# Kernel optimization log

Hardware: AMD Instinct MI355X
Metric: run time of the kernel (lower is better)

The kernel has to match this reference:

```python
import jax, jax.numpy as jnp
import numpy as np

N = 100000   # total atoms
M = 12       # neighbors per atom
C = 2000     # crystals
ORIG = 92    # original atom feature len
NBR = 41     # edge (Gaussian distance) feature len
F = 64       # atom_fea_len
H = 128      # h_fea_len
NCONV = 3
EPS = 1e-5


def setup_inputs() -> dict:
    key = jax.random.key(0)
    ks = jax.random.split(key, 12)
    def w(k, shape, fan_in):
        return (jax.random.normal(k, shape, jnp.float32) / np.sqrt(fan_in)).astype(jnp.float32)
    inp = {}
    inp["atom_fea"] = jax.random.normal(ks[0], (N, ORIG), jnp.float32)
    inp["nbr_fea"] = jax.random.normal(ks[1], (N, M, NBR), jnp.float32)
    inp["nbr_fea_idx"] = jax.random.randint(ks[2], (N, M), 0, N)
    inp["crystal_ids"] = jnp.sort(jax.random.randint(ks[3], (N,), 0, C))
    inp["emb_W"] = w(ks[4], (ORIG, F), ORIG)
    inp["emb_b"] = jnp.zeros((F,), jnp.float32)
    inp["conv_W"] = w(ks[5], (NCONV, 2 * F + NBR, 2 * F), 2 * F + NBR)
    inp["conv_b"] = jnp.zeros((NCONV, 2 * F), jnp.float32)
    inp["bn1_g"] = jnp.ones((NCONV, 2 * F), jnp.float32)
    inp["bn1_b"] = jnp.zeros((NCONV, 2 * F), jnp.float32)
    inp["bn2_g"] = jnp.ones((NCONV, F), jnp.float32)
    inp["bn2_b"] = jnp.zeros((NCONV, F), jnp.float32)
    inp["W3_W"] = w(ks[6], (F, F), F)
    inp["W3_b"] = jnp.zeros((F,), jnp.float32)
    inp["fc_W"] = w(ks[7], (F, H), F)
    inp["fc_b"] = jnp.zeros((H,), jnp.float32)
    inp["out_W"] = w(ks[8], (H, 1), H)
    inp["out_b"] = jnp.zeros((1,), jnp.float32)
    return inp


def _bn(x, g, b):
    # BatchNorm1d in training mode: batch mean, biased variance
    m = jnp.mean(x, axis=0)
    v = jnp.var(x, axis=0)
    return (x - m) * jax.lax.rsqrt(v + EPS) * g + b


def _seg_mean(x, ids, num):
    s = jax.ops.segment_sum(x, ids, num_segments=num)          # [num, F]
    cnt = jax.ops.segment_sum(jnp.ones((x.shape[0], 1), x.dtype), ids, num_segments=num)
    return s / jnp.maximum(cnt, 1.0)


def _conv_layer(x, nbr_fea, nbr_idx, W, b, g1, b1, g2, b2):
    n, m = nbr_idx.shape
    atom_nbr = x[nbr_idx]                                      # [N, M, F] gather
    self_fea = jnp.broadcast_to(x[:, None, :], (n, m, x.shape[1]))
    total = jnp.concatenate([self_fea, atom_nbr, nbr_fea], axis=2)  # [N, M, 2F+NBR]
    gated = total @ W + b                                      # [N, M, 2F]
    gated = _bn(gated.reshape(-1, 2 * F), g1, b1).reshape(n, m, 2 * F)
    nbr_filter = jax.nn.sigmoid(gated[..., :F])
    nbr_core = jnp.tanh(gated[..., F:])
    nbr_sumed = jnp.sum(nbr_filter * nbr_core, axis=1)          # [N, F]
    nbr_sumed = _bn(nbr_sumed, g2, b2)
    return jnp.tanh(x + nbr_sumed)


def reference(atom_fea, nbr_fea, nbr_fea_idx, crystal_ids,
              emb_W, emb_b, conv_W, conv_b, bn1_g, bn1_b, bn2_g, bn2_b,
              W3_W, W3_b, fc_W, fc_b, out_W, out_b):
    x = atom_fea @ emb_W + emb_b                               # [N, F]
    for i in range(NCONV):
        x = _conv_layer(x, nbr_fea, nbr_fea_idx, conv_W[i], conv_b[i],
                        bn1_g[i], bn1_b[i], bn2_g[i], bn2_b[i])
    # pooling(): per-crystal mean expanded back to each atom
    crys_mean = _seg_mean(x, crystal_ids, C)                   # [C, F]
    v_ = crys_mean[crystal_ids]                                # [N, F]
    c = jnp.tanh(v_ @ W3_W + W3_b)                             # [N, F]
    a = jax.nn.sigmoid(jnp.sum(x * c, axis=1, keepdims=True))  # [N, 1]
    crys_fea = _seg_mean(a * x, crystal_ids, C)                # [C, F]
    crys_fea = jax.nn.softplus(crys_fea @ fc_W + fc_b)         # [C, H]
    out = crys_fea @ out_W + out_b                             # [C, 1]
    return out, x
```

## Files before the change

### kernel.cpp

```cpp
#include <hip/hip_runtime.h>
#include <hip/hip_bf16.h>


#define NA    100000
#define MN    12
#define NC    2000
#define ORIGF 92
#define NBRF  41
#define FD    64
#define NBLK  3125
#define EPSF  1e-5f

#define REP28(X) X(0)X(1)X(2)X(3)X(4)X(5)X(6)X(7)X(8)X(9)X(10)X(11)X(12)X(13)X(14)X(15)X(16)X(17)X(18)X(19)X(20)X(21)X(22)X(23)X(24)X(25)X(26)X(27)
#define REP41(X) X(0)X(1)X(2)X(3)X(4)X(5)X(6)X(7)X(8)X(9)X(10)X(11)X(12)X(13)X(14)X(15)X(16)X(17)X(18)X(19)X(20)X(21)X(22)X(23)X(24)X(25)X(26)X(27)X(28)X(29)X(30)X(31)X(32)X(33)X(34)X(35)X(36)X(37)X(38)X(39)X(40)
#define REP64(X) X(0)X(1)X(2)X(3)X(4)X(5)X(6)X(7)X(8)X(9)X(10)X(11)X(12)X(13)X(14)X(15)X(16)X(17)X(18)X(19)X(20)X(21)X(22)X(23)X(24)X(25)X(26)X(27)X(28)X(29)X(30)X(31)X(32)X(33)X(34)X(35)X(36)X(37)X(38)X(39)X(40)X(41)X(42)X(43)X(44)X(45)X(46)X(47)X(48)X(49)X(50)X(51)X(52)X(53)X(54)X(55)X(56)X(57)X(58)X(59)X(60)X(61)X(62)X(63)

typedef const float* fp;

__device__ __forceinline__ float rlf(float v, int q){
  return __int_as_float(__builtin_amdgcn_readlane(__float_as_int(v), q));
}
__device__ __forceinline__ float fsig(float z){
  z = fminf(fmaxf(z, -30.f), 30.f);
  return 1.f / (1.f + __expf(-z));
}
__device__ __forceinline__ float ftanh(float z){
  z = fminf(fmaxf(z, -15.f), 15.f);
  float e = __expf(2.f * z);
  return (e - 1.f) / (e + 1.f);
}

__global__ void zero_kernel(float* __restrict__ p, int n){
  for (int i = blockIdx.x * blockDim.x + threadIdx.x; i < n; i += gridDim.x * blockDim.x)
    p[i] = 0.f;
}

__global__ __launch_bounds__(256, 2) void emb_kernel(
    fp __restrict__ af, fp __restrict__ W, fp __restrict__ b,
    float* __restrict__ x)
{
  const int lane = threadIdx.x & 63, w = threadIdx.x >> 6;
#define EA(k) float wa##k = W[k * FD + lane];
  REP64(EA)
#undef EA
#define EB(k) float wb##k = W[(k + 64) * FD + lane];
  REP28(EB)
#undef EB
  const float bias = b[lane];
  const int base = blockIdx.x * 32 + w * 8;
  #pragma unroll 1
  for (int it = 0; it < 8; ++it){
    const int i = base + it;
    float ev0 = af[i * ORIGF + lane];
    float ev1 = (lane < 28) ? af[i * ORIGF + 64 + lane] : 0.f;
    float acc = bias;
#define FA(k) acc = fmaf(rlf(ev0, k), wa##k, acc);
    REP64(FA)
#undef FA
#define FB(k) acc = fmaf(rlf(ev1, k), wb##k, acc);
    REP28(FB)
#undef FB
    x[i * FD + lane] = acc;
  }
}

__global__ __launch_bounds__(256, 4) void stw_kernel(
    const float* __restrict__ xin, fp __restrict__ W, fp __restrict__ bias,
    float* __restrict__ out)
{
  const int lane = threadIdx.x & 63, w = threadIdx.x >> 6;
  const int ch = (w & 1) * 64 + lane;
#define SW(k) float wv##k = W[k * 128 + ch];
  REP64(SW)
#undef SW
  const float bb = bias ? bias[ch] : 0.f;
  const int base = blockIdx.x * 32 + (w >> 1) * 16;
  #pragma unroll 1
  for (int it = 0; it < 16; ++it){
    const int i = base + it;
    float xv = xin[i * FD + lane];
    float acc = bb;
#define SF(k) acc = fmaf(rlf(xv, k), wv##k, acc);
    REP64(SF)
#undef SF
    out[i * 128 + ch] = acc;
  }
}

__global__ __launch_bounds__(256, 2) void edge_stats_kernel(
    const float* __restrict__ S, const float* __restrict__ T,
    fp __restrict__ nbr, const int* __restrict__ idx,
    fp __restrict__ We, float* __restrict__ p1)
{
  const int lane = threadIdx.x & 63, w = threadIdx.x >> 6;
  const int clo = lane, chi = lane + 64;
#define DW(q) float wlo##q = We[q * 128 + clo], whi##q = We[q * 128 + chi];
  REP41(DW)
#undef DW
  float sum_lo = 0.f, ssq_lo = 0.f, sum_hi = 0.f, ssq_hi = 0.f;
  const int base = blockIdx.x * 32 + w * 8;
  #pragma unroll 1
  for (int it = 0; it < 8; ++it){
    const int i = base + it;
    const float slo = S[i * 128 + clo];
    const float shi = S[i * 128 + chi];
    int kk = (lane < MN) ? idx[i * MN + lane] : 0;
    fp nb = nbr + (size_t)i * (MN * NBRF);
    int k0 = __builtin_amdgcn_readlane(kk, 0);
    float tlo = T[k0 * 128 + clo];
    float thi = T[k0 * 128 + chi];
    float ev  = (lane < NBRF) ? nb[lane] : 0.f;
    #pragma unroll 1
    for (int j = 0; j < MN; j++){
      float tlo_n = 0.f, thi_n = 0.f, ev_n = 0.f;
      if (j + 1 < MN){
        int kn = __builtin_amdgcn_readlane(kk, j + 1);
        tlo_n = T[kn * 128 + clo];
        thi_n = T[kn * 128 + chi];
        ev_n  = (lane < NBRF) ? nb[(j + 1) * NBRF + lane] : 0.f;
      }
      float glo = slo + tlo, ghi = shi + thi;
#define EF(q) { float s_ = rlf(ev, q); glo = fmaf(s_, wlo##q, glo); ghi = fmaf(s_, whi##q, ghi); }
      REP41(EF)
#undef EF
      sum_lo += glo; ssq_lo = fmaf(glo, glo, ssq_lo);
      sum_hi += ghi; ssq_hi = fmaf(ghi, ghi, ssq_hi);
      tlo = tlo_n; thi = thi_n; ev = ev_n;
    }
  }
  __shared__ float red[4 * 512];
  red[w * 512 + 2 * clo    ] = sum_lo;
  red[w * 512 + 2 * clo + 1] = ssq_lo;
  red[w * 512 + 2 * chi    ] = sum_hi;
  red[w * 512 + 2 * chi + 1] = ssq_hi;
  __syncthreads();
  const int t = threadIdx.x;
  const int ch = t & 127, which = t >> 7;
  float v = 0.f;
  #pragma unroll
  for (int ww = 0; ww < 4; ++ww) v += red[ww * 512 + 2 * ch + which];
  p1[blockIdx.x * 256 + t] = v;
}

__global__ __launch_bounds__(256, 2) void edge_stats_store_kernel(
    const float* __restrict__ S, const float* __restrict__ T,
    fp __restrict__ nbr, const int* __restrict__ idx,
    fp __restrict__ We, float* __restrict__ p1, float* __restrict__ gated)
{
  const int lane = threadIdx.x & 63, w = threadIdx.x >> 6;
  const int clo = lane, chi = lane + 64;
#define DW(q) float wlo##q = We[q * 128 + clo], whi##q = We[q * 128 + chi];
  REP41(DW)
#undef DW
  float sum_lo = 0.f, ssq_lo = 0.f, sum_hi = 0.f, ssq_hi = 0.f;
  const int base = blockIdx.x * 32 + w * 8;
  #pragma unroll 1
  for (int it = 0; it < 8; ++it){
    const int i = base + it;
    const float slo = S[i * 128 + clo];
    const float shi = S[i * 128 + chi];
    int kk = (lane < MN) ? idx[i * MN + lane] : 0;
    fp nb = nbr + (size_t)i * (MN * NBRF);
    float* gb = gated + (((size_t)i * MN) << 7) + 2 * lane;
    int k0 = __builtin_amdgcn_readlane(kk, 0);
    float tlo = T[k0 * 128 + clo];
    float thi = T[k0 * 128 + chi];
    float ev  = (lane < NBRF) ? nb[lane] : 0.f;
    #pragma unroll 1
    for (int j = 0; j < MN; j++){
      float tlo_n = 0.f, thi_n = 0.f, ev_n = 0.f;
      if (j + 1 < MN){
        int kn = __builtin_amdgcn_readlane(kk, j + 1);
        tlo_n = T[kn * 128 + clo];
        thi_n = T[kn * 128 + chi];
        ev_n  = (lane < NBRF) ? nb[(j + 1) * NBRF + lane] : 0.f;
      }
      float glo = slo + tlo, ghi = shi + thi;
#define EF(q) { float s_ = rlf(ev, q); glo = fmaf(s_, wlo##q, glo); ghi = fmaf(s_, whi##q, ghi); }
      REP41(EF)
#undef EF
      *(float2*)(gb + ((size_t)j << 7)) = make_float2(glo, ghi);
      sum_lo += glo; ssq_lo = fmaf(glo, glo, ssq_lo);
      sum_hi += ghi; ssq_hi = fmaf(ghi, ghi, ssq_hi);
      tlo = tlo_n; thi = thi_n; ev = ev_n;
    }
  }
  __shared__ float red[4 * 512];
  red[w * 512 + 2 * clo    ] = sum_lo;
  red[w * 512 + 2 * clo + 1] = ssq_lo;
  red[w * 512 + 2 * chi    ] = sum_hi;
  red[w * 512 + 2 * chi + 1] = ssq_hi;
  __syncthreads();
  const int t = threadIdx.x;
  const int ch = t & 127, which = t >> 7;
  float v = 0.f;
  #pragma unroll
  for (int ww = 0; ww < 4; ++ww) v += red[ww * 512 + 2 * ch + which];
  p1[blockIdx.x * 256 + t] = v;
}

__global__ __launch_bounds__(256, 4) void edge_apply_load_kernel(
    const float* __restrict__ gated, const float* __restrict__ ss1,
    float* __restrict__ ns, float* __restrict__ p2)
{
  const int lane = threadIdx.x & 63, w = threadIdx.x >> 6;
  const float sc_lo = ss1[lane],      sh_lo = ss1[128 + lane];
  const float sc_hi = ss1[64 + lane], sh_hi = ss1[192 + lane];
  float sum2 = 0.f, ssq2 = 0.f;
  const int base = blockIdx.x * 32 + w * 8;
  #pragma unroll 1
  for (int it = 0; it < 8; ++it){
    const int i = base + it;
    fp gb = gated + (((size_t)i * MN) << 7) + 2 * lane;
    float acc = 0.f;
    #pragma unroll
    for (int j = 0; j < MN; ++j){
      float2 gv = *(const float2*)(gb + ((size_t)j << 7));
      float filt = fsig(fmaf(gv.x, sc_lo, sh_lo));
      float core = ftanh(fmaf(gv.y, sc_hi, sh_hi));
      acc = fmaf(filt, core, acc);
    }
    ns[i * FD + lane] = acc;
    sum2 += acc; ssq2 = fmaf(acc, acc, ssq2);
  }
  __shared__ float red[4 * 128];
  red[w * 128 + 2 * lane    ] = sum2;
  red[w * 128 + 2 * lane + 1] = ssq2;
  __syncthreads();
  const int t = threadIdx.x;
  if (t < 128){
    const int ch = t & 63, which = t >> 6;
    float v = 0.f;
    #pragma unroll
    for (int ww = 0; ww < 4; ++ww) v += red[ww * 128 + 2 * ch + which];
    p2[blockIdx.x * 128 + t] = v;
  }
}

__global__ __launch_bounds__(256, 2) void edge_apply_kernel(
    const float* __restrict__ S, const float* __restrict__ T,
    fp __restrict__ nbr, const int* __restrict__ idx,
    fp __restrict__ We, const float* __restrict__ ss1,
    float* __restrict__ ns, float* __restrict__ p2)
{
  const int lane = threadIdx.x & 63, w = threadIdx.x >> 6;
  const int clo = lane, chi = lane + 64;
#define DW(q) float wlo##q = We[q * 128 + clo], whi##q = We[q * 128 + chi];
  REP41(DW)
#undef DW
  const float sc_lo = ss1[clo],       sh_lo = ss1[128 + clo];
  const float sc_hi = ss1[chi],       sh_hi = ss1[128 + chi];
  float sum2 = 0.f, ssq2 = 0.f;
  const int base = blockIdx.x * 32 + w * 8;
  #pragma unroll 1
  for (int it = 0; it < 8; ++it){
    const int i = base + it;
    const float slo = S[i * 128 + clo];
    const float shi = S[i * 128 + chi];
    int kk = (lane < MN) ? idx[i * MN + lane] : 0;
    fp nb = nbr + (size_t)i * (MN * NBRF);
    int k0 = __builtin_amdgcn_readlane(kk, 0);
    float tlo = T[k0 * 128 + clo];
    float thi = T[k0 * 128 + chi];
    float ev  = (lane < NBRF) ? nb[lane] : 0.f;
    float acc = 0.f;
    #pragma unroll 1
    for (int j = 0; j < MN; j++){
      float tlo_n = 0.f, thi_n = 0.f, ev_n = 0.f;
      if (j + 1 < MN){
        int kn = __builtin_amdgcn_readlane(kk, j + 1);
        tlo_n = T[kn * 128 + clo];
        thi_n = T[kn * 128 + chi];
        ev_n  = (lane < NBRF) ? nb[(j + 1) * NBRF + lane] : 0.f;
      }
      float glo = slo + tlo, ghi = shi + thi;
#define EF(q) { float s_ = rlf(ev, q); glo = fmaf(s_, wlo##q, glo); ghi = fmaf(s_, whi##q, ghi); }
      REP41(EF)
#undef EF
      float filt = fsig(fmaf(glo, sc_lo, sh_lo));
      float core = ftanh(fmaf(ghi, sc_hi, sh_hi));
      acc = fmaf(filt, core, acc);
      tlo = tlo_n; thi = thi_n; ev = ev_n;
    }
    ns[i * FD + lane] = acc;
    sum2 += acc; ssq2 = fmaf(acc, acc, ssq2);
  }
  __shared__ float red[4 * 128];
  red[w * 128 + 2 * lane    ] = sum2;
  red[w * 128 + 2 * lane + 1] = ssq2;
  __syncthreads();
  const int t = threadIdx.x;
  if (t < 128){
    const int ch = t & 63, which = t >> 6;
    float v = 0.f;
    #pragma unroll
    for (int ww = 0; ww < 4; ++ww) v += red[ww * 128 + 2 * ch + which];
    p2[blockIdx.x * 128 + t] = v;
  }
}

__global__ void reduce_rows_kernel(const float* __restrict__ p, float* __restrict__ accum,
                                   int nrows, int ncols)
{
  const int t = threadIdx.x;
  float a = 0.f;
  for (int r = blockIdx.x; r < nrows; r += gridDim.x) a += p[r * ncols + t];
  atomicAdd(&accum[t], a);
}

__global__ void finalize1_kernel(const float* __restrict__ acc, fp g, fp b,
                                 float* __restrict__ ss1)
{
  const int c = threadIdx.x;
  const float inv = 1.f / 1200000.f;
  float mean = acc[c] * inv;
  float var  = fmaxf(acc[128 + c] * inv - mean * mean, 0.f);
  float sc   = g[c] * rsqrtf(var + EPSF);
  ss1[c] = sc;
  ss1[128 + c] = b[c] - mean * sc;
}

__global__ void finalize2_kernel(const float* __restrict__ acc, fp g, fp b,
                                 float* __restrict__ ss2)
{
  const int c = threadIdx.x;
  const float inv = 1.f / 100000.f;
  float mean = acc[c] * inv;
  float var  = fmaxf(acc[64 + c] * inv - mean * mean, 0.f);
  float sc   = g[c] * rsqrtf(var + EPSF);
  ss2[c] = sc;
  ss2[64 + c] = b[c] - mean * sc;
}

__global__ __launch_bounds__(256) void bn2res_kernel(
    float* __restrict__ x, const float* __restrict__ ns,
    const float* __restrict__ ss2, float* __restrict__ xout)
{
  const int e = (blockIdx.x * 256 + threadIdx.x) * 4;
  const int c = e & 63;
  float4 xv = *(const float4*)(x + e);
  float4 nv = *(const float4*)(ns + e);
  float r0 = ftanh(fmaf(nv.x, ss2[c + 0], ss2[64 + c + 0]) + xv.x);
  float r1 = ftanh(fmaf(nv.y, ss2[c + 1], ss2[64 + c + 1]) + xv.y);
  float r2 = ftanh(fmaf(nv.z, ss2[c + 2], ss2[64 + c + 2]) + xv.z);
  float r3 = ftanh(fmaf(nv.w, ss2[c + 3], ss2[64 + c + 3]) + xv.w);
  *(float4*)(x + e) = make_float4(r0, r1, r2, r3);
  if (xout){
    *(float4*)(xout + e) = make_float4(r0, r1, r2, r3);
  }
}

__global__ __launch_bounds__(256) void pool1_kernel(
    const float* __restrict__ x, const int* __restrict__ cid,
    float* __restrict__ csum, float* __restrict__ ccnt)
{
  const int lane = threadIdx.x & 63, w = threadIdx.x >> 6;
  const int wg = blockIdx.x * 4 + w;
  const int i0 = wg * 64;
  if (i0 >= NA) return;
  const int i1 = min(i0 + 64, NA);
  int cur = -1; float acc = 0.f; int run = 0;
  for (int i = i0; i < i1; ++i){
    int cd = cid[i];
    if (cd != cur){
      if (cur >= 0){
        atomicAdd(&csum[cur * FD + lane], acc);
        if (lane == 0) atomicAdd(&ccnt[cur], (float)run);
      }
      cur = cd; acc = 0.f; run = 0;
    }
    acc += x[i * FD + lane];
    run++;
  }
  if (cur >= 0){
    atomicAdd(&csum[cur * FD + lane], acc);
    if (lane == 0) atomicAdd(&ccnt[cur], (float)run);
  }
}

__global__ void cm3_kernel(const float* __restrict__ csum, const float* __restrict__ ccnt,
                           fp W3, fp b3, float* __restrict__ c3)
{
  const int b = blockIdx.x, t = threadIdx.x;
  __shared__ float mean[64];
  float inv = 1.f / fmaxf(ccnt[b], 1.f);
  mean[t] = csum[b * FD + t] * inv;
  __syncthreads();
  float acc = b3[t];
  #pragma unroll
  for (int k = 0; k < 64; k++) acc = fmaf(mean[k], W3[k * FD + t], acc);
  c3[b * FD + t] = ftanh(acc);
}

__global__ __launch_bounds__(256) void pool2_kernel(
    const float* __restrict__ x, const int* __restrict__ cid,
    const float* __restrict__ c3, float* __restrict__ cfs)
{
  const int lane = threadIdx.x & 63, w = threadIdx.x >> 6;
  const int wg = blockIdx.x * 4 + w;
  const int i0 = wg * 64;
  if (i0 >= NA) return;
  const int i1 = min(i0 + 64, NA);
  int cur = -1; float acc = 0.f;
  for (int i = i0; i < i1; ++i){
    int cd = cid[i];
    if (cd != cur){
      if (cur >= 0) atomicAdd(&cfs[cur * FD + lane], acc);
      cur = cd; acc = 0.f;
    }
    float xv = x[i * FD + lane];
    float p = xv * c3[cd * FD + lane];
    #pragma unroll
    for (int off = 32; off; off >>= 1) p += __shfl_xor(p, off);
    acc = fmaf(fsig(p), xv, acc);
  }
  if (cur >= 0) atomicAdd(&cfs[cur * FD + lane], acc);
}

__global__ void head_kernel(const float* __restrict__ cfs, const float* __restrict__ ccnt,
                            fp fcW, fp fcb, fp oW, fp ob,
                            float* __restrict__ outp)
{
  const int b = blockIdx.x, t = threadIdx.x;
  __shared__ float row[64];
  __shared__ float red[128];
  float inv = 1.f / fmaxf(ccnt[b], 1.f);
  if (t < 64) row[t] = cfs[b * FD + t] * inv;
  __syncthreads();
  float acc = fcb[t];
  #pragma unroll
  for (int k = 0; k < 64; k++) acc = fmaf(row[k], fcW[k * 128 + t], acc);
  float sp = (acc > 20.f) ? acc : log1pf(__expf(acc));
  red[t] = sp * oW[t];
  __syncthreads();
  for (int off = 64; off; off >>= 1){
    if (t < off) red[t] += red[t + off];
    __syncthreads();
  }
  if (t == 0) outp[b] = red[0] + ob[0];
}

static const size_t O_X    = 0;
static const size_t O_S    = 6400000;
static const size_t O_T    = 19200000;
static const size_t O_NS   = 32000000;
static const size_t O_P1   = 38400000;
static const size_t O_P2   = 39200000;
static const size_t O_SS1  = 39600000;
static const size_t O_SS2  = 39600256;
static const size_t O_G1   = 39600384;
static const size_t O_G2   = 39600640;
static const size_t O_CSUM = 39600768;
static const size_t O_CCNT = 39728768;
static const size_t O_C3   = 39730768;
static const size_t O_CFS  = 39858768;
static const size_t O_END  = 39986768;
static const size_t O_GATED= 39986768;
static const size_t O_END2 = 193586768;

extern "C" void kernel_launch(void* const* d_in, const int* in_sizes, int n_in,
                              void* d_out, int out_size, void* d_ws, size_t ws_size,
                              hipStream_t stream)
{
  (void)in_sizes; (void)n_in; (void)out_size;
  if (ws_size < O_END * sizeof(float)) return;
  const bool big = ws_size >= O_END2 * sizeof(float);

  fp atom_fea = (fp)d_in[0];
  fp nbr_fea  = (fp)d_in[1];
  const int* nbr_idx = (const int*)d_in[2];
  const int* cids    = (const int*)d_in[3];
  fp embW = (fp)d_in[4];
  fp embb = (fp)d_in[5];
  fp convW = (fp)d_in[6];
  fp convb = (fp)d_in[7];
  fp bn1g = (fp)d_in[8];
  fp bn1b = (fp)d_in[9];
  fp bn2g = (fp)d_in[10];
  fp bn2b = (fp)d_in[11];
  fp W3W  = (fp)d_in[12];
  fp W3b  = (fp)d_in[13];
  fp fcW  = (fp)d_in[14];
  fp fcb  = (fp)d_in[15];
  fp oW   = (fp)d_in[16];
  fp ob   = (fp)d_in[17];

  float* out_head = (float*)d_out;
  float* out_x    = out_head + NC;

  float* W  = (float*)d_ws;
  float* x    = W + O_X;
  float* S    = W + O_S;
  float* T    = W + O_T;
  float* ns   = W + O_NS;
  float* p1   = W + O_P1;
  float* p2   = W + O_P2;
  float* ss1  = W + O_SS1;
  float* ss2  = W + O_SS2;
  float* g1s  = W + O_G1;
  float* g2s  = W + O_G2;
  float* csum = W + O_CSUM;
  float* ccnt = W + O_CCNT;
  float* c3   = W + O_C3;
  float* cfs  = W + O_CFS;
  float* gated= W + O_GATED;

  zero_kernel<<<128, 256, 0, stream>>>(csum, 386000);

  emb_kernel<<<NBLK, 256, 0, stream>>>(atom_fea, embW, embb, x);

  for (int l = 0; l < 3; ++l){
    fp Wl = convW + (size_t)l * 169 * 128;
    stw_kernel<<<NBLK, 256, 0, stream>>>(x, Wl,            convb + l * 128, S);
    stw_kernel<<<NBLK, 256, 0, stream>>>(x, Wl + 64 * 128, (fp)nullptr,     T);
    zero_kernel<<<1, 256, 0, stream>>>(g1s, 384);
    if (big){
      edge_stats_store_kernel<<<NBLK, 256, 0, stream>>>(S, T, nbr_fea, nbr_idx, Wl + 128 * 128, p1, gated);
      reduce_rows_kernel<<<64, 256, 0, stream>>>(p1, g1s, NBLK, 256);
      finalize1_kernel<<<1, 128, 0, stream>>>(g1s, bn1g + l * 128, bn1b + l * 128, ss1);
      edge_apply_load_kernel<<<NBLK, 256, 0, stream>>>(gated, ss1, ns, p2);
    } else {
      edge_stats_kernel<<<NBLK, 256, 0, stream>>>(S, T, nbr_fea, nbr_idx, Wl + 128 * 128, p1);
      reduce_rows_kernel<<<64, 256, 0, stream>>>(p1, g1s, NBLK, 256);
      finalize1_kernel<<<1, 128, 0, stream>>>(g1s, bn1g + l * 128, bn1b + l * 128, ss1);
      edge_apply_kernel<<<NBLK, 256, 0, stream>>>(S, T, nbr_fea, nbr_idx, Wl + 128 * 128, ss1, ns, p2);
    }
    reduce_rows_kernel<<<64, 128, 0, stream>>>(p2, g2s, NBLK, 128);
    finalize2_kernel<<<1, 64, 0, stream>>>(g2s, bn2g + l * 64, bn2b + l * 64, ss2);
    bn2res_kernel<<<6250, 256, 0, stream>>>(x, ns, ss2, (l == 2) ? out_x : (float*)nullptr);
  }

  pool1_kernel<<<391, 256, 0, stream>>>(x, cids, csum, ccnt);
  cm3_kernel<<<NC, 64, 0, stream>>>(csum, ccnt, W3W, W3b, c3);
  pool2_kernel<<<391, 256, 0, stream>>>(x, cids, c3, cfs);
  head_kernel<<<NC, 128, 0, stream>>>(cfs, ccnt, fcW, fcb, oW, ob, out_head);
}
```

Measured before the change: 2.548 ms.

## Split edge GEMV channels across warps to halve registers and raise occupancy

Each wavefront in the edge stats/store kernel now handles one 64-channel half instead of both, so it keeps 41 weights in registers instead of 82. Launch bounds go from 2 to 4 blocks per SM, and each wave pair covers 16 atoms instead of 8. The gated buffer layout changes from interleaved lo/hi float2 to planar halves, and the apply kernel now reads it as two scalar loads. In exchange, the S/T gathers, index loads and lane broadcasts of edge features are now done by two waves instead of one.

```diff
diff --git a/kernel.cpp b/kernel.cpp
--- a/kernel.cpp
+++ b/kernel.cpp
@@ -142,60 +142,57 @@
   p1[blockIdx.x * 256 + t] = v;
 }
 
-__global__ __launch_bounds__(256, 2) void edge_stats_store_kernel(
+__global__ __launch_bounds__(256, 4) void edge_stats_store_kernel(
     const float* __restrict__ S, const float* __restrict__ T,
     fp __restrict__ nbr, const int* __restrict__ idx,
     fp __restrict__ We, float* __restrict__ p1, float* __restrict__ gated)
 {
   const int lane = threadIdx.x & 63, w = threadIdx.x >> 6;
-  const int clo = lane, chi = lane + 64;
-#define DW(q) float wlo##q = We[q * 128 + clo], whi##q = We[q * 128 + chi];
+  const int half = w & 1;
+  const int ch = half * 64 + lane;
+#define DW(q) float wv##q = We[q * 128 + ch];
   REP41(DW)
 #undef DW
-  float sum_lo = 0.f, ssq_lo = 0.f, sum_hi = 0.f, ssq_hi = 0.f;
-  const int base = blockIdx.x * 32 + w * 8;
+#define PIN(q) asm volatile("" : "+v"(wv##q));
+  REP41(PIN)
+#undef PIN
+  float sum = 0.f, ssq = 0.f;
+  const int base = blockIdx.x * 32 + (w >> 1) * 16;
   #pragma unroll 1
-  for (int it = 0; it < 8; ++it){
+  for (int it = 0; it < 16; ++it){
     const int i = base + it;
-    const float slo = S[i * 128 + clo];
-    const float shi = S[i * 128 + chi];
+    const float sv = S[i * 128 + ch];
     int kk = (lane < MN) ? idx[i * MN + lane] : 0;
     fp nb = nbr + (size_t)i * (MN * NBRF);
-    float* gb = gated + (((size_t)i * MN) << 7) + 2 * lane;
+    float* gb = gated + (((size_t)i * MN) << 7) + ch;
     int k0 = __builtin_amdgcn_readlane(kk, 0);
-    float tlo = T[k0 * 128 + clo];
-    float thi = T[k0 * 128 + chi];
-    float ev  = (lane < NBRF) ? nb[lane] : 0.f;
+    float tv = T[k0 * 128 + ch];
+    float ev = (lane < NBRF) ? nb[lane] : 0.f;
     #pragma unroll 1
     for (int j = 0; j < MN; j++){
-      float tlo_n = 0.f, thi_n = 0.f, ev_n = 0.f;
+      float tv_n = 0.f, ev_n = 0.f;
       if (j + 1 < MN){
         int kn = __builtin_amdgcn_readlane(kk, j + 1);
-        tlo_n = T[kn * 128 + clo];
-        thi_n = T[kn * 128 + chi];
-        ev_n  = (lane < NBRF) ? nb[(j + 1) * NBRF + lane] : 0.f;
+        tv_n = T[kn * 128 + ch];
+        ev_n = (lane < NBRF) ? nb[(j + 1) * NBRF + lane] : 0.f;
       }
-      float glo = slo + tlo, ghi = shi + thi;
-#define EF(q) { float s_ = rlf(ev, q); glo = fmaf(s_, wlo##q, glo); ghi = fmaf(s_, whi##q, ghi); }
+      float g = sv + tv;
+#define EF(q) g = fmaf(rlf(ev, q), wv##q, g);
       REP41(EF)
 #undef EF
-      *(float2*)(gb + ((size_t)j << 7)) = make_float2(glo, ghi);
-      sum_lo += glo; ssq_lo = fmaf(glo, glo, ssq_lo);
-      sum_hi += ghi; ssq_hi = fmaf(ghi, ghi, ssq_hi);
-      tlo = tlo_n; thi = thi_n; ev = ev_n;
-    }
-  }
-  __shared__ float red[4 * 512];
-  red[w * 512 + 2 * clo    ] = sum_lo;
-  red[w * 512 + 2 * clo + 1] = ssq_lo;
-  red[w * 512 + 2 * chi    ] = sum_hi;
-  red[w * 512 + 2 * chi + 1] = ssq_hi;
+      gb[(size_t)j << 7] = g;
+      sum += g; ssq = fmaf(g, g, ssq);
+      tv = tv_n; ev = ev_n;
+    }
+  }
+  __shared__ float red[4 * 128];
+  red[w * 128 + 2 * lane    ] = sum;
+  red[w * 128 + 2 * lane + 1] = ssq;
   __syncthreads();
   const int t = threadIdx.x;
-  const int ch = t & 127, which = t >> 7;
-  float v = 0.f;
-  #pragma unroll
-  for (int ww = 0; ww < 4; ++ww) v += red[ww * 512 + 2 * ch + which];
+  const int c = t & 127, which = t >> 7;
+  const int h = c >> 6, cl = c & 63;
+  float v = red[h * 128 + 2 * cl + which] + red[(h + 2) * 128 + 2 * cl + which];
   p1[blockIdx.x * 256 + t] = v;
 }
 
@@ -211,13 +208,14 @@
   #pragma unroll 1
   for (int it = 0; it < 8; ++it){
     const int i = base + it;
-    fp gb = gated + (((size_t)i * MN) << 7) + 2 * lane;
+    fp gb = gated + (((size_t)i * MN) << 7);
     float acc = 0.f;
     #pragma unroll
     for (int j = 0; j < MN; ++j){
-      float2 gv = *(const float2*)(gb + ((size_t)j << 7));
-      float filt = fsig(fmaf(gv.x, sc_lo, sh_lo));
-      float core = ftanh(fmaf(gv.y, sc_hi, sh_hi));
+      float glo = gb[(j << 7) + lane];
+      float ghi = gb[(j << 7) + 64 + lane];
+      float filt = fsig(fmaf(glo, sc_lo, sh_lo));
+      float core = ftanh(fmaf(ghi, sc_hi, sh_hi));
       acc = fmaf(filt, core, acc);
     }
     ns[i * FD + lane] = acc;
```

Measured after the change: 2.869 ms. 1.13x slower.

## Stage edge features in LDS and process four neighbors per batch

Applied to the files above, without the earlier changes.

The edge-stats kernel now copies each atom's 12x41 edge-feature block into shared memory and reads the values as LDS broadcasts, replacing per-coefficient readlane broadcasts. It processes four neighbors per inner step, issuing the four T gathers together to get more memory-level parallelism and ILP. The gated buffer layout changes from interleaved lo/hi float2 to split lo and hi halves, and the apply kernel is updated to match. The costs are higher register pressure from four accumulator pairs, and the LDS write-then-read relies only on a waitcnt with no barrier, which is fine within a single wave.

```diff
diff --git a/kernel.cpp b/kernel.cpp
--- a/kernel.cpp
+++ b/kernel.cpp
@@ -152,6 +152,7 @@
 #define DW(q) float wlo##q = We[q * 128 + clo], whi##q = We[q * 128 + chi];
   REP41(DW)
 #undef DW
+  __shared__ float elds[4][MN * NBRF];
   float sum_lo = 0.f, ssq_lo = 0.f, sum_hi = 0.f, ssq_hi = 0.f;
   const int base = blockIdx.x * 32 + w * 8;
   #pragma unroll 1
@@ -161,28 +162,43 @@
     const float shi = S[i * 128 + chi];
     int kk = (lane < MN) ? idx[i * MN + lane] : 0;
     fp nb = nbr + (size_t)i * (MN * NBRF);
-    float* gb = gated + (((size_t)i * MN) << 7) + 2 * lane;
-    int k0 = __builtin_amdgcn_readlane(kk, 0);
-    float tlo = T[k0 * 128 + clo];
-    float thi = T[k0 * 128 + chi];
-    float ev  = (lane < NBRF) ? nb[lane] : 0.f;
+    #pragma unroll
+    for (int r = 0; r < 7; ++r) elds[w][r * 64 + lane] = nb[r * 64 + lane];
+    if (lane < MN * NBRF - 448) elds[w][448 + lane] = nb[448 + lane];
+    asm volatile("s_waitcnt lgkmcnt(0)" ::: "memory");
     #pragma unroll 1
-    for (int j = 0; j < MN; j++){
-      float tlo_n = 0.f, thi_n = 0.f, ev_n = 0.f;
-      if (j + 1 < MN){
-        int kn = __builtin_amdgcn_readlane(kk, j + 1);
-        tlo_n = T[kn * 128 + clo];
-        thi_n = T[kn * 128 + chi];
-        ev_n  = (lane < NBRF) ? nb[(j + 1) * NBRF + lane] : 0.f;
-      }
-      float glo = slo + tlo, ghi = shi + thi;
-#define EF(q) { float s_ = rlf(ev, q); glo = fmaf(s_, wlo##q, glo); ghi = fmaf(s_, whi##q, ghi); }
+    for (int jg = 0; jg < MN / 4; ++jg){
+      const int j0 = jg * 4;
+      int k0 = __builtin_amdgcn_readlane(kk, j0);
+      int k1 = __builtin_amdgcn_readlane(kk, j0 + 1);
+      int k2 = __builtin_amdgcn_readlane(kk, j0 + 2);
+      int k3 = __builtin_amdgcn_readlane(kk, j0 + 3);
+      float g0lo = slo + T[k0 * 128 + clo], g0hi = shi + T[k0 * 128 + chi];
+      float g1lo = slo + T[k1 * 128 + clo], g1hi = shi + T[k1 * 128 + chi];
+      float g2lo = slo + T[k2 * 128 + clo], g2hi = shi + T[k2 * 128 + chi];
+      float g3lo = slo + T[k3 * 128 + clo], g3hi = shi + T[k3 * 128 + chi];
+      const float* eb = &elds[w][j0 * NBRF];
+#define EF(q) { float e0_ = eb[q]; float e1_ = eb[NBRF + q]; \
+                float e2_ = eb[2 * NBRF + q]; float e3_ = eb[3 * NBRF + q]; \
+                g0lo = fmaf(e0_, wlo##q, g0lo); g0hi = fmaf(e0_, whi##q, g0hi); \
+                g1lo = fmaf(e1_, wlo##q, g1lo); g1hi = fmaf(e1_, whi##q, g1hi); \
+                g2lo = fmaf(e2_, wlo##q, g2lo); g2hi = fmaf(e2_, whi##q, g2hi); \
+                g3lo = fmaf(e3_, wlo##q, g3lo); g3hi = fmaf(e3_, whi##q, g3hi); }
       REP41(EF)
 #undef EF
-      *(float2*)(gb + ((size_t)j << 7)) = make_float2(glo, ghi);
-      sum_lo += glo; ssq_lo = fmaf(glo, glo, ssq_lo);
-      sum_hi += ghi; ssq_hi = fmaf(ghi, ghi, ssq_hi);
-      tlo = tlo_n; thi = thi_n; ev = ev_n;
+      float* gb = gated + (((size_t)(i * MN + j0)) << 7);
+      gb[lane]       = g0lo; gb[64 + lane]  = g0hi;
+      gb[128 + lane] = g1lo; gb[192 + lane] = g1hi;
+      gb[256 + lane] = g2lo; gb[320 + lane] = g2hi;
+      gb[384 + lane] = g3lo; gb[448 + lane] = g3hi;
+      sum_lo += g0lo; ssq_lo = fmaf(g0lo, g0lo, ssq_lo);
+      sum_hi += g0hi; ssq_hi = fmaf(g0hi, g0hi, ssq_hi);
+      sum_lo += g1lo; ssq_lo = fmaf(g1lo, g1lo, ssq_lo);
+      sum_hi += g1hi; ssq_hi = fmaf(g1hi, g1hi, ssq_hi);
+      sum_lo += g2lo; ssq_lo = fmaf(g2lo, g2lo, ssq_lo);
+      sum_hi += g2hi; ssq_hi = fmaf(g2hi, g2hi, ssq_hi);
+      sum_lo += g3lo; ssq_lo = fmaf(g3lo, g3lo, ssq_lo);
+      sum_hi += g3hi; ssq_hi = fmaf(g3hi, g3hi, ssq_hi);
     }
   }
   __shared__ float red[4 * 512];
@@ -211,13 +227,14 @@
   #pragma unroll 1
   for (int it = 0; it < 8; ++it){
     const int i = base + it;
-    fp gb = gated + (((size_t)i * MN) << 7) + 2 * lane;
+    fp gb = gated + (((size_t)i * MN) << 7);
     float acc = 0.f;
     #pragma unroll
     for (int j = 0; j < MN; ++j){
-      float2 gv = *(const float2*)(gb + ((size_t)j << 7));
-      float filt = fsig(fmaf(gv.x, sc_lo, sh_lo));
-      float core = ftanh(fmaf(gv.y, sc_hi, sh_hi));
+      float glo = gb[(j << 7) + lane];
+      float ghi = gb[(j << 7) + 64 + lane];
+      float filt = fsig(fmaf(glo, sc_lo, sh_lo));
+      float core = ftanh(fmaf(ghi, sc_hi, sh_hi));
       acc = fmaf(filt, core, acc);
     }
     ns[i * FD + lane] = acc;
```

After: 2.442 ms. -4.1%, faster.
